# Kernel optimization log

Measured on AMD Instinct MI355X. Metric: run time of the kernel, lower is better.

## Reference

```python
import jax, jax.numpy as jnp
import numpy as np

# Config: 8 AllInOneBlocks, total_dim=4 (3 + pad_dim 1), subnet hidden 128
L = 8          # inn_coupling_blocks
D = 4          # total_dim = 3 + pad_dim
H = 128        # inn_subnet_hidden
B = 524288     # batch of XYZ colors
CLAMP = 2.0    # FrEIA affine_clamping default


def setup_inputs() -> dict:
    key = jax.random.key(0)
    ks = jax.random.split(key, 10)
    f32 = jnp.float32
    XYZ = jax.random.normal(ks[0], (B, 3), dtype=f32)
    # Stacked per-block subnet params: Linear(2,H) -> GELU -> Linear(H,H) -> GELU -> Linear(H,4)
    W1 = (jax.random.normal(ks[1], (L, H, 2), dtype=f32) / np.sqrt(2.0).astype(np.float32))
    b1 = 0.05 * jax.random.normal(ks[2], (L, H), dtype=f32)
    W2 = (jax.random.normal(ks[3], (L, H, H), dtype=f32) / np.sqrt(float(H)).astype(np.float32))
    b2 = 0.05 * jax.random.normal(ks[4], (L, H), dtype=f32)
    W3 = (jax.random.normal(ks[5], (L, D, H), dtype=f32) / np.sqrt(float(H)).astype(np.float32))
    b3 = 0.05 * jax.random.normal(ks[6], (L, D), dtype=f32)
    # Global affine (SOFTPLUS type): param init so 0.1*softplus_{beta=0.5}(g) == 1
    g0 = np.float32(2.0 * np.log(np.exp(5.0) - 1.0))
    g = jnp.full((L, D), g0, dtype=f32) + 0.1 * jax.random.normal(ks[7], (L, D), dtype=f32)
    off = 0.05 * jax.random.normal(ks[8], (L, D), dtype=f32)
    # permute_soft=True: fixed random SO(D) matrix per block (QR of gaussian, det fixed to +1)
    A = jax.random.normal(ks[9], (L, D, D), dtype=f32)
    Q, R = jnp.linalg.qr(A)
    Q = Q * jnp.sign(jnp.diagonal(R, axis1=1, axis2=2))[:, None, :]
    det = jnp.linalg.det(Q)
    Q = Q.at[:, :, 0].multiply(det[:, None])
    return {"XYZ": XYZ, "W1": W1, "b1": b1, "W2": W2, "b2": b2,
            "W3": W3, "b3": b3, "g": g, "off": off, "P": Q.astype(f32)}


def _inn_forward(XYZ, W1, b1, W2, b2, W3, b3, g, off, P):
    x = jnp.pad(XYZ, ((0, 0), (0, 1)))  # _pad: (B,3) -> (B,4), 4th dim zero
    lj0 = jnp.zeros(XYZ.shape[0], dtype=XYZ.dtype)

    def step(carry, p):
        x, lj = carry
        w1, c1, w2, c2, w3, c3, gg, oo, pp = p
        x1, x2 = x[:, :2], x[:, 2:]                       # splits = [2, 2]
        h = jax.nn.gelu(x1 @ w1.T + c1, approximate=False)
        h = jax.nn.gelu(h @ w2.T + c2, approximate=False)
        a = (h @ w3.T + c3) * 0.1                         # FrEIA scales coupling coeffs by 0.1
        s = CLAMP * jnp.tanh(a[:, :2])
        x2n = x2 * jnp.exp(s) + a[:, 2:]                  # affine coupling
        scale = 0.2 * jax.nn.softplus(0.5 * gg)           # 0.1 * Softplus(beta=0.5)
        y = (jnp.concatenate([x1, x2n], axis=1) * scale + oo) @ pp.T  # global affine + soft perm
        lj = lj + jnp.sum(s, axis=1) + jnp.sum(jnp.log(scale))
        return (y, lj), None

    (z, log_jac), _ = jax.lax.scan(step, (x, lj0), (W1, b1, W2, b2, W3, b3, g, off, P))
    return z, log_jac


def reference(XYZ, W1, b1, W2, b2, W3, b3, g, off, P):
    z, _ = _inn_forward(XYZ, W1, b1, W2, b2, W3, b3, g, off, P)
    return z[:, :3]
```

## Files before the change

kernel.cpp:

```cpp
#include <hip/hip_runtime.h>
#include <hip/hip_bf16.h>


#define MEMBAR() asm volatile("" ::: "memory")

typedef float    f32x4 __attribute__((ext_vector_type(4)));
typedef short    s16x4 __attribute__((ext_vector_type(4), may_alias));
typedef int      i32x4 __attribute__((ext_vector_type(4), may_alias));
typedef _Float16 h16x2 __attribute__((ext_vector_type(2)));
typedef _Float16 h16x8 __attribute__((ext_vector_type(8)));

#define MFMA(a,b,c) __builtin_amdgcn_mfma_f32_16x16x32_f16((a),(b),(c),0,0,0)

#define LBYTES 46080
#define HSTRIDE 304

__device__ __forceinline__ h16x2 pkrtz(float a, float b){
  auto t = __builtin_amdgcn_cvt_pkrtz(a, b);
  h16x2 r; __builtin_memcpy(&r, &t, 4); return r;
}
__device__ __forceinline__ unsigned pkh(float a, float b){
  auto t = __builtin_amdgcn_cvt_pkrtz(a, b);
  unsigned r; __builtin_memcpy(&r, &t, 4); return r;
}

__device__ __forceinline__ h16x2 gelu_pk(h16x2 x){
  const h16x2 Q   = {(_Float16)0.25f,      (_Float16)0.25f};
  const h16x2 CLO = {(_Float16)-0.9375f,   (_Float16)-0.9375f};
  const h16x2 CHI = {(_Float16)0.9375f,    (_Float16)0.9375f};
  const h16x2 D4  = {(_Float16)2.639031f,  (_Float16)2.639031f};
  const h16x2 D3  = {(_Float16)-6.920503f, (_Float16)-6.920503f};
  const h16x2 D2  = {(_Float16)7.180759f,  (_Float16)7.180759f};
  const h16x2 D1  = {(_Float16)-3.960064f, (_Float16)-3.960064f};
  const h16x2 D0  = {(_Float16)1.590628f,  (_Float16)1.590628f};
  const h16x2 H   = {(_Float16)0.5f,       (_Float16)0.5f};
  h16x2 xs = x * Q;
  xs = __builtin_elementwise_max(xs, CLO);
  xs = __builtin_elementwise_min(xs, CHI);
  h16x2 t = xs * xs;
  h16x2 s = t*D4 + D3;
  s = s*t + D2;
  s = s*t + D1;
  s = s*t + D0;
  h16x2 phi = xs*s + H;
  return x * phi;
}

__device__ __forceinline__ void gelu4(const f32x4 c, unsigned& w0, unsigned& w1){
  h16x2 p0 = gelu_pk(pkrtz(c[0], c[1]));
  h16x2 p1 = gelu_pk(pkrtz(c[2], c[3]));
  __builtin_memcpy(&w0, &p0, 4);
  __builtin_memcpy(&w1, &p1, 4);
}

__global__ void prepack(const float* __restrict__ W1, const float* __restrict__ b1,
                        const float* __restrict__ W2, const float* __restrict__ b2,
                        const float* __restrict__ W3, const float* __restrict__ b3,
                        const float* __restrict__ gg, const float* __restrict__ off,
                        const float* __restrict__ Pm, unsigned char* __restrict__ ws)
{
  int t = blockIdx.x * 256 + threadIdx.x;
  if (t >= 8 * 45 * 64) return;
  int l    = t / (45 * 64);
  int rem  = t % (45 * 64);
  int f    = rem / 64;
  int lane = rem % 64;
  int p = lane & 15, g = lane >> 4;
  unsigned char* lb = ws + l * LBYTES;

  if (f < 32) {
    int mf = f >> 2, kc = f & 3;
    const float* rw = W2 + l*16384 + (16*mf + p)*128 + 32*kc + 8*g;
    f32x4 u0 = *(const f32x4*)rw;
    f32x4 u1 = *(const f32x4*)(rw + 4);
    i32x4 w;
    w[0] = (int)pkh(u0[0], u0[1]); w[1] = (int)pkh(u0[2], u0[3]);
    w[2] = (int)pkh(u1[0], u1[1]); w[3] = (int)pkh(u1[2], u1[3]);
    *(i32x4*)(lb + f*1024 + lane*16) = w;
  } else if (f == 32) {
    if (lane < 16) {
      int kc = lane >> 2, gq = lane & 3;
      unsigned w0p[4], w1p[4], bbp[4];
      #pragma unroll
      for (int j2 = 0; j2 < 4; ++j2) {
        int n0 = 32*kc + 8*gq + 2*j2;
        int n1 = n0 + 1;
        w0p[j2] = pkh(W1[l*256 + n0*2 + 0], W1[l*256 + n1*2 + 0]);
        w1p[j2] = pkh(W1[l*256 + n0*2 + 1], W1[l*256 + n1*2 + 1]);
        bbp[j2] = pkh(b1[l*128 + n0],       b1[l*128 + n1]);
      }
      unsigned char* dst = lb + 32*1024 + lane*48;
      i32x4 a, b, c;
      #pragma unroll
      for (int q = 0; q < 4; ++q) { a[q]=(int)w0p[q]; b[q]=(int)w1p[q]; c[q]=(int)bbp[q]; }
      *(i32x4*)(dst)      = a;
      *(i32x4*)(dst + 16) = b;
      *(i32x4*)(dst + 32) = c;
    }
  } else if (f >= 40 && f < 44) {
    int kc = f - 40;
    i32x4 w = (i32x4){0,0,0,0};
    if (p < 4) {
      const float* rw = W3 + l*512 + p*128 + 8*g + 32*kc;
      f32x4 u0 = *(const f32x4*)(rw);
      f32x4 u1 = *(const f32x4*)(rw + 4);
      w[0] = (int)pkh(0.1f*u0[0], 0.1f*u0[1]); w[1] = (int)pkh(0.1f*u0[2], 0.1f*u0[3]);
      w[2] = (int)pkh(0.1f*u1[0], 0.1f*u1[1]); w[3] = (int)pkh(0.1f*u1[2], 0.1f*u1[3]);
    }
    *(i32x4*)(lb + f*1024 + lane*16) = w;
  } else if (f == 44) {
    float* sm = (float*)(lb + 45056);
    if (lane < 16) {
      int j = lane & 3;
      float scl = 0.2f * log1pf(expf(0.5f * gg[l*4 + j]));
      sm[lane] = Pm[l*16 + lane] * scl;
    } else if (lane < 20) {
      int i = lane - 16; float acc = 0.f;
      #pragma unroll
      for (int j = 0; j < 4; ++j) acc += Pm[l*16 + i*4 + j] * off[l*4 + j];
      sm[16 + i] = acc;
    } else if (lane < 24) {
      sm[lane] = 0.1f * b3[l*4 + (lane - 20)];
    }
    sm[24 + lane]      = b2[l*128 + lane];
    sm[24 + 64 + lane] = b2[l*128 + 64 + lane];
  }
}

__global__ __launch_bounds__(256, 3) void inn_main(
    const float* __restrict__ XYZ,
    const unsigned char* __restrict__ ws,
    float* __restrict__ outp)
{
  __shared__ __align__(16) unsigned char lds[4*5888];

  const int tid  = threadIdx.x;
  const int wid  = tid >> 6;
  const int lane = tid & 63;
  const int p    = lane & 15;
  const int g    = lane >> 4;
  unsigned char* hb = lds + wid*5888;
  float* xs = (float*)(hb + 4864);
  const long base_pt = (long)blockIdx.x*256 + wid*64;
  const f32x4 z4 = {0.f,0.f,0.f,0.f};
  const unsigned loff = (unsigned)lane * 16u;

  if (lane < 16) {
    for (int s = 0; s < 4; ++s) {
      long pt = base_pt + s*16 + p;
      f32x4 v;
      v[0]=XYZ[pt*3+0]; v[1]=XYZ[pt*3+1]; v[2]=XYZ[pt*3+2]; v[3]=0.f;
      *(f32x4*)&xs[(s*16+p)*4] = v;
    }
  }
  MEMBAR();

  for (int l = 0; l < 8; ++l) {
    const unsigned char* lb = ws + l * LBYTES;
    const float* sm = (const float*)(lb + 45056);
    f32x4 b3v = z4;
    if (g == 0) b3v = *(const f32x4*)(sm + 20);

    h16x2 X0[4], X1[4];
    #pragma unroll
    for (int t = 0; t < 4; ++t) {
      f32x4 xv = *(const f32x4*)&xs[(t*16+p)*4];
      X0[t] = pkrtz(xv[0], xv[0]);
      X1[t] = pkrtz(xv[1], xv[1]);
    }
    h16x8 bfr1[4][4];
    #pragma unroll
    for (int kc = 0; kc < 4; ++kc) {
      const unsigned char* wd = lb + 32*1024 + (kc*4 + g)*48;
      h16x2 w0p[4], w1p[4], bbp[4];
      __builtin_memcpy(w0p, wd,      16);
      __builtin_memcpy(w1p, wd + 16, 16);
      __builtin_memcpy(bbp, wd + 32, 16);
      #pragma unroll
      for (int t = 0; t < 4; ++t) {
        h16x2 hp[4];
        #pragma unroll
        for (int j2 = 0; j2 < 4; ++j2) {
          h16x2 v = w0p[j2]*X0[t] + w1p[j2]*X1[t] + bbp[j2];
          hp[j2] = gelu_pk(v);
        }
        __builtin_memcpy(&bfr1[kc][t], hp, 16);
      }
    }

    f32x4 c3[4];
    #pragma unroll
    for (int t = 0; t < 4; ++t) c3[t] = b3v;
    #pragma unroll
    for (int mfp = 0; mfp < 4; ++mfp) {
      f32x4 bv0 = *(const f32x4*)(sm + 24 + 16*(2*mfp)   + 4*g);
      f32x4 bv1 = *(const f32x4*)(sm + 24 + 16*(2*mfp+1) + 4*g);
      f32x4 c2a[4], c2b[4];
      #pragma unroll
      for (int t = 0; t < 4; ++t) { c2a[t] = bv0; c2b[t] = bv1; }
      #pragma unroll
      for (int kc = 0; kc < 4; ++kc) {
        h16x8 af0 = *(const h16x8*)(lb + ((2*mfp)*4   + kc)*1024 + loff);
        h16x8 af1 = *(const h16x8*)(lb + ((2*mfp+1)*4 + kc)*1024 + loff);
        #pragma unroll
        for (int t = 0; t < 4; ++t) {
          c2a[t] = MFMA(af0, bfr1[kc][t], c2a[t]);
          c2b[t] = MFMA(af1, bfr1[kc][t], c2b[t]);
        }
      }
      h16x8 a3 = *(const h16x8*)(lb + (40 + mfp)*1024 + loff);
      #pragma unroll
      for (int t = 0; t < 4; ++t) {
        i32x4 w; unsigned w0,w1,w2,w3;
        gelu4(c2a[t], w0, w1); gelu4(c2b[t], w2, w3);
        w[0]=(int)w0; w[1]=(int)w1; w[2]=(int)w2; w[3]=(int)w3;
        *(i32x4*)(hb + p*HSTRIDE + (4*t + g)*16) = w;
      }
      #pragma unroll
      for (int t = 0; t < 4; ++t) {
        const unsigned char* ra = hb + p*HSTRIDE + (4*t + 2*(g & 1))*16 + (g >> 1)*8;
        s16x4 lo = *(const s16x4*)(ra);
        s16x4 hi = *(const s16x4*)(ra + 16);
        h16x8 b;
        __builtin_memcpy(&b, &lo, 8);
        __builtin_memcpy(((char*)&b)+8, &hi, 8);
        c3[t] = MFMA(a3, b, c3[t]);
      }
    }

    f32x4 ps0 = *(const f32x4*)(sm + 0);
    f32x4 ps1 = *(const f32x4*)(sm + 4);
    f32x4 ps2 = *(const f32x4*)(sm + 8);
    f32x4 ps3 = *(const f32x4*)(sm + 12);
    f32x4 pb  = *(const f32x4*)(sm + 16);
    int addr = p << 2;
    #pragma unroll
    for (int t = 0; t < 4; ++t) {
      f32x4 xv = *(const f32x4*)&xs[(t*16+p)*4];
      float a0 = __int_as_float(__builtin_amdgcn_ds_bpermute(addr, __float_as_int(c3[t][0])));
      float a1 = __int_as_float(__builtin_amdgcn_ds_bpermute(addr, __float_as_int(c3[t][1])));
      float a2 = __int_as_float(__builtin_amdgcn_ds_bpermute(addr, __float_as_int(c3[t][2])));
      float a3f= __int_as_float(__builtin_amdgcn_ds_bpermute(addr, __float_as_int(c3[t][3])));
      float t0 = __builtin_amdgcn_rcpf(1.f + __builtin_amdgcn_exp2f(2.8853901f * a0));
      float t1 = __builtin_amdgcn_rcpf(1.f + __builtin_amdgcn_exp2f(2.8853901f * a1));
      float e0 = __builtin_amdgcn_exp2f(__builtin_fmaf(-5.7707802f, t0, 2.8853901f));
      float e1 = __builtin_amdgcn_exp2f(__builtin_fmaf(-5.7707802f, t1, 2.8853901f));
      float v2 = __builtin_fmaf(xv[2], e0, a2);
      float v3 = __builtin_fmaf(xv[3], e1, a3f);
      f32x4 y;
      y[0] = __builtin_fmaf(ps0[0], xv[0], __builtin_fmaf(ps0[1], xv[1],
             __builtin_fmaf(ps0[2], v2, __builtin_fmaf(ps0[3], v3, pb[0]))));
      y[1] = __builtin_fmaf(ps1[0], xv[0], __builtin_fmaf(ps1[1], xv[1],
             __builtin_fmaf(ps1[2], v2, __builtin_fmaf(ps1[3], v3, pb[1]))));
      y[2] = __builtin_fmaf(ps2[0], xv[0], __builtin_fmaf(ps2[1], xv[1],
             __builtin_fmaf(ps2[2], v2, __builtin_fmaf(ps2[3], v3, pb[2]))));
      y[3] = __builtin_fmaf(ps3[0], xv[0], __builtin_fmaf(ps3[1], xv[1],
             __builtin_fmaf(ps3[2], v2, __builtin_fmaf(ps3[3], v3, pb[3]))));
      if (g == 0) *(f32x4*)&xs[(t*16+p)*4] = y;
    }
  }

  if (lane < 16) {
    for (int s = 0; s < 4; ++s) {
      long pt = base_pt + s*16 + p;
      f32x4 xv = *(const f32x4*)&xs[(s*16+p)*4];
      outp[pt*3+0] = xv[0];
      outp[pt*3+1] = xv[1];
      outp[pt*3+2] = xv[2];
    }
  }
}

extern "C" void kernel_launch(void* const* d_in, const int* in_sizes, int n_in,
                              void* d_out, int out_size, void* d_ws, size_t ws_size,
                              hipStream_t stream)
{
  const float* XYZ = (const float*)d_in[0];
  const float* W1  = (const float*)d_in[1];
  const float* b1  = (const float*)d_in[2];
  const float* W2  = (const float*)d_in[3];
  const float* b2  = (const float*)d_in[4];
  const float* W3  = (const float*)d_in[5];
  const float* b3  = (const float*)d_in[6];
  const float* g   = (const float*)d_in[7];
  const float* off = (const float*)d_in[8];
  const float* P   = (const float*)d_in[9];
  unsigned char* ws = (unsigned char*)d_ws;

  prepack<<<90, 256, 0, stream>>>(W1, b1, W2, b2, W3, b3, g, off, P, ws);

  int Bn = in_sizes[0] / 3;
  int nblocks = Bn / 256;
  inn_main<<<nblocks, 256, 0, stream>>>(XYZ, ws, (float*)d_out);
}
```

Before: 313.1 us.

## Fold GELU input scale into weights and spread coupling epilogue across all lanes

Pre-scales W1, b1, W2 and b2 by 0.25 during prepacking, so the packed-fp16 GELU no longer multiplies its input by a quarter. The polynomial coefficients are rescaled to match. The coupling and permutation epilogue now has each lane group handle a different 16-point tile, picked with lane selects, instead of every lane computing all four tiles and only group 0 writing. This removes redundant transcendental and FMA work per layer, at the cost of some selects and a slight change to fp16 rounding.

```diff
diff --git a/kernel.cpp b/kernel.cpp
--- a/kernel.cpp
+++ b/kernel.cpp
@@ -24,31 +24,29 @@
   unsigned r; __builtin_memcpy(&r, &t, 4); return r;
 }
 
-__device__ __forceinline__ h16x2 gelu_pk(h16x2 x){
-  const h16x2 Q   = {(_Float16)0.25f,      (_Float16)0.25f};
-  const h16x2 CLO = {(_Float16)-0.9375f,   (_Float16)-0.9375f};
-  const h16x2 CHI = {(_Float16)0.9375f,    (_Float16)0.9375f};
-  const h16x2 D4  = {(_Float16)2.639031f,  (_Float16)2.639031f};
-  const h16x2 D3  = {(_Float16)-6.920503f, (_Float16)-6.920503f};
-  const h16x2 D2  = {(_Float16)7.180759f,  (_Float16)7.180759f};
-  const h16x2 D1  = {(_Float16)-3.960064f, (_Float16)-3.960064f};
-  const h16x2 D0  = {(_Float16)1.590628f,  (_Float16)1.590628f};
-  const h16x2 H   = {(_Float16)0.5f,       (_Float16)0.5f};
-  h16x2 xs = x * Q;
-  xs = __builtin_elementwise_max(xs, CLO);
-  xs = __builtin_elementwise_min(xs, CHI);
-  h16x2 t = xs * xs;
-  h16x2 s = t*D4 + D3;
-  s = s*t + D2;
-  s = s*t + D1;
-  s = s*t + D0;
-  h16x2 phi = xs*s + H;
-  return x * phi;
+__device__ __forceinline__ h16x2 gelu_pk4(h16x2 xin){
+  const h16x2 CLO = {(_Float16)-0.9375f,    (_Float16)-0.9375f};
+  const h16x2 CHI = {(_Float16)0.9375f,     (_Float16)0.9375f};
+  const h16x2 E4  = {(_Float16)10.556124f,  (_Float16)10.556124f};
+  const h16x2 E3  = {(_Float16)-27.682012f, (_Float16)-27.682012f};
+  const h16x2 E2  = {(_Float16)28.723036f,  (_Float16)28.723036f};
+  const h16x2 E1  = {(_Float16)-15.840256f, (_Float16)-15.840256f};
+  const h16x2 E0  = {(_Float16)6.362512f,   (_Float16)6.362512f};
+  const h16x2 H2  = {(_Float16)2.0f,        (_Float16)2.0f};
+  h16x2 xq = __builtin_elementwise_max(xin, CLO);
+  xq = __builtin_elementwise_min(xq, CHI);
+  h16x2 t = xq * xq;
+  h16x2 s = t*E4 + E3;
+  s = s*t + E2;
+  s = s*t + E1;
+  s = s*t + E0;
+  h16x2 inner = xq*s + H2;
+  return xin * inner;
 }
 
 __device__ __forceinline__ void gelu4(const f32x4 c, unsigned& w0, unsigned& w1){
-  h16x2 p0 = gelu_pk(pkrtz(c[0], c[1]));
-  h16x2 p1 = gelu_pk(pkrtz(c[2], c[3]));
+  h16x2 p0 = gelu_pk4(pkrtz(c[0], c[1]));
+  h16x2 p1 = gelu_pk4(pkrtz(c[2], c[3]));
   __builtin_memcpy(&w0, &p0, 4);
   __builtin_memcpy(&w1, &p1, 4);
 }
@@ -74,8 +72,8 @@
     f32x4 u0 = *(const f32x4*)rw;
     f32x4 u1 = *(const f32x4*)(rw + 4);
     i32x4 w;
-    w[0] = (int)pkh(u0[0], u0[1]); w[1] = (int)pkh(u0[2], u0[3]);
-    w[2] = (int)pkh(u1[0], u1[1]); w[3] = (int)pkh(u1[2], u1[3]);
+    w[0] = (int)pkh(0.25f*u0[0], 0.25f*u0[1]); w[1] = (int)pkh(0.25f*u0[2], 0.25f*u0[3]);
+    w[2] = (int)pkh(0.25f*u1[0], 0.25f*u1[1]); w[3] = (int)pkh(0.25f*u1[2], 0.25f*u1[3]);
     *(i32x4*)(lb + f*1024 + lane*16) = w;
   } else if (f == 32) {
     if (lane < 16) {
@@ -85,9 +83,9 @@
       for (int j2 = 0; j2 < 4; ++j2) {
         int n0 = 32*kc + 8*gq + 2*j2;
         int n1 = n0 + 1;
-        w0p[j2] = pkh(W1[l*256 + n0*2 + 0], W1[l*256 + n1*2 + 0]);
-        w1p[j2] = pkh(W1[l*256 + n0*2 + 1], W1[l*256 + n1*2 + 1]);
-        bbp[j2] = pkh(b1[l*128 + n0],       b1[l*128 + n1]);
+        w0p[j2] = pkh(0.25f*W1[l*256 + n0*2 + 0], 0.25f*W1[l*256 + n1*2 + 0]);
+        w1p[j2] = pkh(0.25f*W1[l*256 + n0*2 + 1], 0.25f*W1[l*256 + n1*2 + 1]);
+        bbp[j2] = pkh(0.25f*b1[l*128 + n0],       0.25f*b1[l*128 + n1]);
       }
       unsigned char* dst = lb + 32*1024 + lane*48;
       i32x4 a, b, c;
@@ -122,8 +120,8 @@
     } else if (lane < 24) {
       sm[lane] = 0.1f * b3[l*4 + (lane - 20)];
     }
-    sm[24 + lane]      = b2[l*128 + lane];
-    sm[24 + 64 + lane] = b2[l*128 + 64 + lane];
+    sm[24 + lane]      = 0.25f * b2[l*128 + lane];
+    sm[24 + 64 + lane] = 0.25f * b2[l*128 + 64 + lane];
   }
 }
 
@@ -182,7 +180,7 @@
         #pragma unroll
         for (int j2 = 0; j2 < 4; ++j2) {
           h16x2 v = w0p[j2]*X0[t] + w1p[j2]*X1[t] + bbp[j2];
-          hp[j2] = gelu_pk(v);
+          hp[j2] = gelu_pk4(v);
         }
         __builtin_memcpy(&bfr1[kc][t], hp, 16);
       }
@@ -234,19 +232,28 @@
     f32x4 ps3 = *(const f32x4*)(sm + 12);
     f32x4 pb  = *(const f32x4*)(sm + 16);
     int addr = p << 2;
+    f32x4 av[4];
     #pragma unroll
     for (int t = 0; t < 4; ++t) {
-      f32x4 xv = *(const f32x4*)&xs[(t*16+p)*4];
-      float a0 = __int_as_float(__builtin_amdgcn_ds_bpermute(addr, __float_as_int(c3[t][0])));
-      float a1 = __int_as_float(__builtin_amdgcn_ds_bpermute(addr, __float_as_int(c3[t][1])));
-      float a2 = __int_as_float(__builtin_amdgcn_ds_bpermute(addr, __float_as_int(c3[t][2])));
-      float a3f= __int_as_float(__builtin_amdgcn_ds_bpermute(addr, __float_as_int(c3[t][3])));
-      float t0 = __builtin_amdgcn_rcpf(1.f + __builtin_amdgcn_exp2f(2.8853901f * a0));
-      float t1 = __builtin_amdgcn_rcpf(1.f + __builtin_amdgcn_exp2f(2.8853901f * a1));
+      #pragma unroll
+      for (int i = 0; i < 4; ++i)
+        av[t][i] = __int_as_float(__builtin_amdgcn_ds_bpermute(addr, __float_as_int(c3[t][i])));
+    }
+    f32x4 as;
+    #pragma unroll
+    for (int i = 0; i < 4; ++i) {
+      float v01 = (g & 1) ? av[1][i] : av[0][i];
+      float v23 = (g & 1) ? av[3][i] : av[2][i];
+      as[i] = (g & 2) ? v23 : v01;
+    }
+    {
+      f32x4 xv = *(const f32x4*)&xs[(g*16+p)*4];
+      float t0 = __builtin_amdgcn_rcpf(1.f + __builtin_amdgcn_exp2f(2.8853901f * as[0]));
+      float t1 = __builtin_amdgcn_rcpf(1.f + __builtin_amdgcn_exp2f(2.8853901f * as[1]));
       float e0 = __builtin_amdgcn_exp2f(__builtin_fmaf(-5.7707802f, t0, 2.8853901f));
       float e1 = __builtin_amdgcn_exp2f(__builtin_fmaf(-5.7707802f, t1, 2.8853901f));
-      float v2 = __builtin_fmaf(xv[2], e0, a2);
-      float v3 = __builtin_fmaf(xv[3], e1, a3f);
+      float v2 = __builtin_fmaf(xv[2], e0, as[2]);
+      float v3 = __builtin_fmaf(xv[3], e1, as[3]);
       f32x4 y;
       y[0] = __builtin_fmaf(ps0[0], xv[0], __builtin_fmaf(ps0[1], xv[1],
              __builtin_fmaf(ps0[2], v2, __builtin_fmaf(ps0[3], v3, pb[0]))));
@@ -256,8 +263,9 @@
              __builtin_fmaf(ps2[2], v2, __builtin_fmaf(ps2[3], v3, pb[2]))));
       y[3] = __builtin_fmaf(ps3[0], xv[0], __builtin_fmaf(ps3[1], xv[1],
              __builtin_fmaf(ps3[2], v2, __builtin_fmaf(ps3[3], v3, pb[3]))));
-      if (g == 0) *(f32x4*)&xs[(t*16+p)*4] = y;
-    }
+      *(f32x4*)&xs[(g*16+p)*4] = y;
+    }
+    MEMBAR();
   }
 
   if (lane < 16) {
```

Result: faster. 295.3 us (-5.7%).
